# Optimization experiments

Measured on AMD Instinct MI355X. Metric: run time of the kernel, lower is better.

Reference implementation:

```python
import jax, jax.numpy as jnp
import numpy as np

NUM_BINS = 256
BN_EPS = 1e-5


def setup_inputs() -> dict:
    key = jax.random.key(0)
    ks = jax.random.split(key, 16)
    B, C, H, W = 16, 64, 256, 256
    x = jax.random.uniform(ks[0], (B, C, H, W), dtype=jnp.float32) * 255.0
    return {
        "x": x,
        "conv1_w": jax.random.normal(ks[1], (C, C), dtype=jnp.float32) * 0.05,
        "conv1_b": jax.random.normal(ks[2], (C,), dtype=jnp.float32) * 0.05,
        "bn1_gamma": jax.random.uniform(ks[3], (C,), dtype=jnp.float32) + 0.5,
        "bn1_beta": jax.random.normal(ks[4], (C,), dtype=jnp.float32) * 0.05,
        "bn1_mean": jax.random.normal(ks[5], (C,), dtype=jnp.float32) * 0.05,
        "bn1_var": jax.random.uniform(ks[6], (C,), dtype=jnp.float32) + 0.5,
        "conv2_w": jax.random.normal(ks[7], (1, C), dtype=jnp.float32) * 0.05,
        "conv2_b": jax.random.normal(ks[8], (1,), dtype=jnp.float32) * 0.05,
        "bn2_gamma": jax.random.uniform(ks[9], (1,), dtype=jnp.float32) + 0.5,
        "bn2_beta": jax.random.normal(ks[10], (1,), dtype=jnp.float32) * 0.05,
        "bn2_mean": jax.random.normal(ks[11], (1,), dtype=jnp.float32) * 0.05,
        "bn2_var": jax.random.uniform(ks[12], (1,), dtype=jnp.float32) + 0.5,
    }


def _histc_argmax(x):
    # Replicates torch.histc(v, bins=NUM_BINS, min=0, max=255) per (b, c)
    # followed by argmax over bins. Out-of-range values are ignored by histc.
    B, C, H, W = x.shape
    flat = x.reshape(B * C, H * W)
    in_range = (flat >= 0.0) & (flat <= 255.0)
    # histc bin index: floor((v - min) * bins / (max - min)); v == max -> last bin
    idx = jnp.clip((flat * (NUM_BINS / 255.0)).astype(jnp.int32), 0, NUM_BINS - 1)
    rows = jnp.arange(B * C)[:, None]
    hist = jnp.zeros((B * C, NUM_BINS), dtype=jnp.float32).at[rows, idx].add(
        in_range.astype(jnp.float32)
    )
    return hist.argmax(axis=-1).reshape(B, C)  # [B, C] dominant bin indices


def _bn(a, gamma, beta, mean, var):
    inv = gamma * jax.lax.rsqrt(var + BN_EPS)
    return a * inv[None, :, None, None] + (beta - mean * inv)[None, :, None, None]


def reference(x, conv1_w, conv1_b, bn1_gamma, bn1_beta, bn1_mean, bn1_var,
              conv2_w, conv2_b, bn2_gamma, bn2_beta, bn2_mean, bn2_var):
    bin_size = 256 // NUM_BINS  # == 1 for default num_bins
    dominant = _histc_argmax(x)  # [B, C]
    # per-pixel bin index: torch's x.float() // bin_size then .long()
    pixel_bins = jnp.floor(x / bin_size).astype(jnp.int32)  # [B, C, H, W]
    att = (pixel_bins != dominant[:, :, None, None]).astype(x.dtype)
    # conv1 (1x1) -> bn1 -> relu
    a = jnp.einsum('bchw,oc->bohw', att, conv1_w) + conv1_b[None, :, None, None]
    a = jax.nn.relu(_bn(a, bn1_gamma, bn1_beta, bn1_mean, bn1_var))
    # conv2 (1x1, C->1) -> bn2 -> sigmoid
    a = jnp.einsum('bchw,oc->bohw', a, conv2_w) + conv2_b[None, :, None, None]
    a = jax.nn.sigmoid(_bn(a, bn2_gamma, bn2_beta, bn2_mean, bn2_var))
    return x * a
```

## Files before the change

kernel.cpp:

```cpp
#include <hip/hip_runtime.h>
#include <stdint.h>

#define CCH 64
#define HWPIX 65536
#define NBINS 256

typedef float f4 __attribute__((ext_vector_type(4)));


__global__ __launch_bounds__(64) void precomp_kernel(
    const float* __restrict__ w1, const float* __restrict__ b1,
    const float* __restrict__ g1, const float* __restrict__ be1,
    const float* __restrict__ m1, const float* __restrict__ v1,
    const float* __restrict__ w2, const float* __restrict__ b2,
    const float* __restrict__ g2, const float* __restrict__ be2,
    const float* __restrict__ m2, const float* __restrict__ v2,
    float* __restrict__ ws)
{
    int o = threadIdx.x;
    float inv1 = g1[o] * rsqrtf(v1[o] + 1e-5f);
    float S = 0.f;
    for (int c = 0; c < CCH; ++c) S += w1[o * CCH + c];
    float beta1p = be1[o] - m1[o] * inv1;
    float base_pre = (S + b1[o]) * inv1 + beta1p;
    for (int c = 0; c < CCH; ++c) ws[1024 + o * CCH + c] = w1[o * CCH + c] * inv1;
    ws[5120 + o] = base_pre;
    float w2o = w2[o];
    ws[5184 + o] = w2o;
    float t = fmaxf(base_pre, 0.f) * w2o;
    #pragma unroll
    for (int off = 32; off > 0; off >>= 1) t += __shfl_down(t, off, 64);
    if (o == 0) {
        float inv2 = g2[0] * rsqrtf(v2[0] + 1e-5f);
        float beta2p = be2[0] - m2[0] * inv2;
        float z = (t + b2[0]) * inv2 + beta2p;
        ws[5248] = inv2;
        ws[5249] = beta2p;
        ws[5250] = b2[0];
        ws[5251] = 1.f / (1.f + expf(-z));
    }
    __syncthreads();
    {
        int c = o;
        float t1 = 0.f;
        for (int oo = 0; oo < CCH; ++oo) {
            float acc = ws[5120 + oo] - ws[1024 + oo * CCH + c];
            t1 += fmaxf(acc, 0.f) * ws[5184 + oo];
        }
        float z = (t1 + ws[5250]) * ws[5248] + ws[5249];
        ws[5312 + c] = 1.f / (1.f + expf(-z));
    }
}

__global__ __launch_bounds__(64) void precomp2_kernel(float* __restrict__ ws)
{
    int c1 = blockIdx.x, c2 = threadIdx.x;
    float t = 0.f;
    for (int o = 0; o < CCH; ++o) {
        float acc = ws[5120 + o] - ws[1024 + o * CCH + c1] - ws[1024 + o * CCH + c2];
        t += fmaxf(acc, 0.f) * ws[5184 + o];
    }
    float z = (t + ws[5250]) * ws[5248] + ws[5249];
    ws[8192 + c1 * CCH + c2] = 1.f / (1.f + expf(-z));
}

__global__ __launch_bounds__(256) void hist_kernel(
    const float* __restrict__ x, int* __restrict__ dom)
{
    __shared__ unsigned h[16][NBINS + 1];
    __shared__ unsigned long long red[NBINS];
    int tid = threadIdx.x;
    const float4* xp = (const float4*)(x + (size_t)blockIdx.x * HWPIX);

    for (int i = tid; i < 16 * (NBINS + 1); i += 256) ((unsigned*)h)[i] = 0;
    __syncthreads();

    unsigned* hmine = h[tid >> 4];
    const float scale = 256.0f / 255.0f;
    #pragma unroll 4
    for (int t = 0; t < HWPIX / 4 / 256; ++t) {
        float4 v = xp[t * 256 + tid];
        float vv[4] = {v.x, v.y, v.z, v.w};
        #pragma unroll
        for (int j = 0; j < 4; ++j) {
            float f = vv[j];
            if (f >= 0.f && f <= 255.f) {
                int bi = (int)(f * scale);
                bi = bi > NBINS - 1 ? NBINS - 1 : bi;
                atomicAdd(&hmine[bi], 1u);
            }
        }
    }
    __syncthreads();

    unsigned cnt = 0;
    #pragma unroll
    for (int k = 0; k < 16; ++k) cnt += h[k][tid];
    red[tid] = ((unsigned long long)cnt << 32) | (unsigned)(NBINS - 1 - tid);
    __syncthreads();
    #pragma unroll
    for (int s = 128; s > 0; s >>= 1) {
        if (tid < s) {
            unsigned long long a = red[tid], b = red[tid + s];
            red[tid] = a > b ? a : b;
        }
        __syncthreads();
    }
    if (tid == 0) dom[blockIdx.x] = (NBINS - 1) - (int)(red[0] & 0xffffffffu);
}

__global__ __launch_bounds__(256, 8) void main_kernel(
    const float* __restrict__ x, const float* __restrict__ ws,
    const int* __restrict__ dom, float* __restrict__ out)
{
    __shared__ __align__(16) float tile[CCH][68];
    __shared__ unsigned pm[4][CCH];
    __shared__ float ss[CCH];
    __shared__ float df[CCH];

    int tid = threadIdx.x;
    int b = blockIdx.x >> 10;
    int p04 = (blockIdx.x & 1023) << 4;

    if (tid < CCH) df[tid] = (float)dom[b * CCH + tid];

    const f4* xb4 = (const f4*)(x + ((size_t)b << 22));
    #pragma unroll
    for (int k = 0; k < 4; ++k) {
        int id = (k << 8) + tid;
        int c = id >> 4, col = id & 15;
        f4 v = xb4[((size_t)c << 14) + p04 + col];
        *(f4*)&tile[c][col << 2] = v;
    }
    __syncthreads();

    {
        int part = tid >> 6, px = tid & 63;
        unsigned mloc = 0;
        #pragma unroll
        for (int cc = 0; cc < 16; ++cc) {
            int c = (part << 4) | cc;
            float v = tile[c][px];
            float d = df[c];
            mloc |= (unsigned)(v >= d && v < d + 1.0f) << cc;
        }
        pm[part][px] = mloc;
    }
    __syncthreads();

    if (tid < CCH) {
        int px = tid;
        unsigned long long m = (unsigned long long)pm[0][px]
            | ((unsigned long long)pm[1][px] << 16)
            | ((unsigned long long)pm[2][px] << 32)
            | ((unsigned long long)pm[3][px] << 48);
        float s;
        if (m == 0ull) {
            s = ws[5251];
        } else {
            int c1 = __builtin_ctzll(m);
            unsigned long long r1 = m & (m - 1);
            if (r1 == 0ull) {
                s = ws[5312 + c1];
            } else {
                int c2 = __builtin_ctzll(r1);
                unsigned long long r2 = r1 & (r1 - 1);
                if (r2 == 0ull) {
                    s = ws[8192 + (c1 << 6) + c2];
                } else {
                    float t = 0.f;
                    for (int o = 0; o < CCH; ++o) {
                        float acc = ws[5120 + o];
                        unsigned long long mm = m;
                        const float* row = ws + 1024 + (o << 6);
                        while (mm) {
                            int c = __builtin_ctzll(mm);
                            mm &= mm - 1;
                            acc -= row[c];
                        }
                        t += fmaxf(acc, 0.f) * ws[5184 + o];
                    }
                    float z = (t + ws[5250]) * ws[5248] + ws[5249];
                    s = 1.f / (1.f + expf(-z));
                }
            }
        }
        ss[px] = s;
    }
    __syncthreads();

    f4* ob4 = (f4*)(out + ((size_t)b << 22));
    #pragma unroll
    for (int k = 0; k < 4; ++k) {
        int id = (k << 8) + tid;
        int c = id >> 4, col = id & 15;
        f4 v = *(const f4*)&tile[c][col << 2];
        f4 sv = *(const f4*)&ss[col << 2];
        v *= sv;
        __builtin_nontemporal_store(v, &ob4[((size_t)c << 14) + p04 + col]);
    }
}

extern "C" void kernel_launch(void* const* d_in, const int* in_sizes, int n_in,
                              void* d_out, int out_size, void* d_ws, size_t ws_size,
                              hipStream_t stream) {
    const float* x   = (const float*)d_in[0];
    const float* w1  = (const float*)d_in[1];
    const float* b1  = (const float*)d_in[2];
    const float* g1  = (const float*)d_in[3];
    const float* be1 = (const float*)d_in[4];
    const float* m1  = (const float*)d_in[5];
    const float* v1  = (const float*)d_in[6];
    const float* w2  = (const float*)d_in[7];
    const float* b2  = (const float*)d_in[8];
    const float* g2  = (const float*)d_in[9];
    const float* be2 = (const float*)d_in[10];
    const float* m2  = (const float*)d_in[11];
    const float* v2  = (const float*)d_in[12];

    float* ws  = (float*)d_ws;
    int*   dom = (int*)d_ws;
    float* outp = (float*)d_out;

    int B = in_sizes[0] / (CCH * HWPIX);

    precomp_kernel<<<1, 64, 0, stream>>>(w1, b1, g1, be1, m1, v1,
                                         w2, b2, g2, be2, m2, v2, ws);
    precomp2_kernel<<<CCH, 64, 0, stream>>>(ws);
    hist_kernel<<<B * CCH, 256, 0, stream>>>(x, dom);
    main_kernel<<<B * (HWPIX / 64), 256, 0, stream>>>(x, ws, dom, outp);
}
```

Baseline: 167.9 us.

## Make main kernel persistent over 8 chunks with double-buffered async LDS loads

Each block of the main kernel now handles 8 consecutive 64-pixel chunks instead of one, loading the next chunk straight into LDS with global_load_lds while the current chunk is processed. The channel-mask computation is also reworked so 64 threads each scan all 64 channels in one pass, replacing the two-stage partial-mask reduction. The intent is to hide global load latency and spread per-block setup cost over more work. The cost is 8x fewer blocks (2048), which may reduce occupancy and latency hiding across the GPU, and most lanes sit idle during the mask phase.

```diff
diff --git a/kernel.cpp b/kernel.cpp
--- a/kernel.cpp
+++ b/kernel.cpp
@@ -6,6 +6,11 @@
 #define NBINS 256
 
 typedef float f4 __attribute__((ext_vector_type(4)));
+
+#define GLDS16(gp, lp)                                                        \
+    __builtin_amdgcn_global_load_lds(                                         \
+        (const __attribute__((address_space(1))) uint32_t*)(gp),              \
+        (__attribute__((address_space(3))) uint32_t*)(lp), 16, 0, 0)
 
 
 __global__ __launch_bounds__(64) void precomp_kernel(
@@ -109,95 +114,105 @@
     if (tid == 0) dom[blockIdx.x] = (NBINS - 1) - (int)(red[0] & 0xffffffffu);
 }
 
-__global__ __launch_bounds__(256, 8) void main_kernel(
+__global__ __launch_bounds__(256) void main_kernel(
     const float* __restrict__ x, const float* __restrict__ ws,
     const int* __restrict__ dom, float* __restrict__ out)
 {
-    __shared__ __align__(16) float tile[CCH][68];
-    __shared__ unsigned pm[4][CCH];
-    __shared__ float ss[CCH];
+    __shared__ __align__(16) float tile[2][CCH * 64];
+    __shared__ float ss[64];
     __shared__ float df[CCH];
 
     int tid = threadIdx.x;
-    int b = blockIdx.x >> 10;
-    int p04 = (blockIdx.x & 1023) << 4;
-
-    if (tid < CCH) df[tid] = (float)dom[b * CCH + tid];
-
-    const f4* xb4 = (const f4*)(x + ((size_t)b << 22));
+    int img = blockIdx.x >> 7;
+    int c0  = (blockIdx.x & 127) << 3;
+
+    const f4* xb4 = (const f4*)(x + ((size_t)img << 22));
+    f4*       ob4 = (f4*)(out + ((size_t)img << 22));
+
     #pragma unroll
     for (int k = 0; k < 4; ++k) {
         int id = (k << 8) + tid;
         int c = id >> 4, col = id & 15;
-        f4 v = xb4[((size_t)c << 14) + p04 + col];
-        *(f4*)&tile[c][col << 2] = v;
-    }
-    __syncthreads();
-
-    {
-        int part = tid >> 6, px = tid & 63;
-        unsigned mloc = 0;
+        GLDS16(xb4 + ((size_t)c << 14) + (c0 << 4) + col, &tile[0][id << 2]);
+    }
+    if (tid < CCH) df[tid] = (float)dom[img * CCH + tid];
+    __syncthreads();
+
+    for (int i = 0; i < 8; ++i) {
+        int cur = i & 1;
+        int j = c0 + i;
+        if (i < 7) {
+            int jn = j + 1;
+            #pragma unroll
+            for (int k = 0; k < 4; ++k) {
+                int id = (k << 8) + tid;
+                int c = id >> 4, col = id & 15;
+                GLDS16(xb4 + ((size_t)c << 14) + (jn << 4) + col,
+                       &tile[cur ^ 1][id << 2]);
+            }
+            asm volatile("s_waitcnt vmcnt(4)" ::: "memory");
+        } else {
+            asm volatile("s_waitcnt vmcnt(0)" ::: "memory");
+        }
+        __builtin_amdgcn_s_barrier();
+
+        if ((tid & 63) < 16) {
+            int px = ((tid >> 6) << 4) | (tid & 15);
+            const float* tc = &tile[cur][0];
+            unsigned long long m = 0ull;
+            #pragma unroll
+            for (int c = 0; c < CCH; ++c) {
+                float v = tc[(c << 6) | px];
+                float d = df[c];
+                m |= (unsigned long long)(v >= d && v < d + 1.0f) << c;
+            }
+            float s;
+            if (m == 0ull) {
+                s = ws[5251];
+            } else {
+                int c1 = __builtin_ctzll(m);
+                unsigned long long r1 = m & (m - 1);
+                if (r1 == 0ull) {
+                    s = ws[5312 + c1];
+                } else {
+                    int c2 = __builtin_ctzll(r1);
+                    unsigned long long r2 = r1 & (r1 - 1);
+                    if (r2 == 0ull) {
+                        s = ws[8192 + (c1 << 6) + c2];
+                    } else {
+                        float t = 0.f;
+                        for (int o = 0; o < CCH; ++o) {
+                            float acc = ws[5120 + o];
+                            unsigned long long mm = m;
+                            const float* row = ws + 1024 + (o << 6);
+                            while (mm) {
+                                int c = __builtin_ctzll(mm);
+                                mm &= mm - 1;
+                                acc -= row[c];
+                            }
+                            t += fmaxf(acc, 0.f) * ws[5184 + o];
+                        }
+                        float z = (t + ws[5250]) * ws[5248] + ws[5249];
+                        s = 1.f / (1.f + expf(-z));
+                    }
+                }
+            }
+            ss[px] = s;
+        }
+        asm volatile("s_waitcnt lgkmcnt(0)" ::: "memory");
+        __builtin_amdgcn_s_barrier();
+
         #pragma unroll
-        for (int cc = 0; cc < 16; ++cc) {
-            int c = (part << 4) | cc;
-            float v = tile[c][px];
-            float d = df[c];
-            mloc |= (unsigned)(v >= d && v < d + 1.0f) << cc;
-        }
-        pm[part][px] = mloc;
-    }
-    __syncthreads();
-
-    if (tid < CCH) {
-        int px = tid;
-        unsigned long long m = (unsigned long long)pm[0][px]
-            | ((unsigned long long)pm[1][px] << 16)
-            | ((unsigned long long)pm[2][px] << 32)
-            | ((unsigned long long)pm[3][px] << 48);
-        float s;
-        if (m == 0ull) {
-            s = ws[5251];
-        } else {
-            int c1 = __builtin_ctzll(m);
-            unsigned long long r1 = m & (m - 1);
-            if (r1 == 0ull) {
-                s = ws[5312 + c1];
-            } else {
-                int c2 = __builtin_ctzll(r1);
-                unsigned long long r2 = r1 & (r1 - 1);
-                if (r2 == 0ull) {
-                    s = ws[8192 + (c1 << 6) + c2];
-                } else {
-                    float t = 0.f;
-                    for (int o = 0; o < CCH; ++o) {
-                        float acc = ws[5120 + o];
-                        unsigned long long mm = m;
-                        const float* row = ws + 1024 + (o << 6);
-                        while (mm) {
-                            int c = __builtin_ctzll(mm);
-                            mm &= mm - 1;
-                            acc -= row[c];
-                        }
-                        t += fmaxf(acc, 0.f) * ws[5184 + o];
-                    }
-                    float z = (t + ws[5250]) * ws[5248] + ws[5249];
-                    s = 1.f / (1.f + expf(-z));
-                }
-            }
-        }
-        ss[px] = s;
-    }
-    __syncthreads();
-
-    f4* ob4 = (f4*)(out + ((size_t)b << 22));
-    #pragma unroll
-    for (int k = 0; k < 4; ++k) {
-        int id = (k << 8) + tid;
-        int c = id >> 4, col = id & 15;
-        f4 v = *(const f4*)&tile[c][col << 2];
-        f4 sv = *(const f4*)&ss[col << 2];
-        v *= sv;
-        __builtin_nontemporal_store(v, &ob4[((size_t)c << 14) + p04 + col]);
+        for (int k = 0; k < 4; ++k) {
+            int id = (k << 8) + tid;
+            int c = id >> 4, col = id & 15;
+            f4 v = *(const f4*)&tile[cur][id << 2];
+            f4 sv = *(const f4*)&ss[col << 2];
+            v *= sv;
+            __builtin_nontemporal_store(v, &ob4[((size_t)c << 14) + (j << 4) + col]);
+        }
+        asm volatile("s_waitcnt lgkmcnt(0)" ::: "memory");
+        __builtin_amdgcn_s_barrier();
     }
 }
 
@@ -228,5 +243,5 @@
                                          w2, b2, g2, be2, m2, v2, ws);
     precomp2_kernel<<<CCH, 64, 0, stream>>>(ws);
     hist_kernel<<<B * CCH, 256, 0, stream>>>(x, dom);
-    main_kernel<<<B * (HWPIX / 64), 256, 0, stream>>>(x, ws, dom, outp);
-}
+    main_kernel<<<B * 128, 256, 0, stream>>>(x, ws, dom, outp);
+}
```

Result: slower. 266.6 us (+58.7%).

## Keep pixel data in registers and reverse block order in main kernel

Applied to the files above, without the earlier changes.

The main kernel no longer stages the 64x64 input tile in shared memory. Each thread now holds four float4 values in registers, builds per-channel match bitmasks, and ORs them through small shared arrays before scaling and storing directly from registers. Blocks are also processed in reverse order, so the last images read by the histogram kernel are likely still in cache (L2/MALL). This cuts shared-memory traffic and LDS footprint, and may improve cache reuse of x, in exchange for more registers per thread.

```diff
diff --git a/kernel.cpp b/kernel.cpp
--- a/kernel.cpp
+++ b/kernel.cpp
@@ -6,6 +6,7 @@
 #define NBINS 256
 
 typedef float f4 __attribute__((ext_vector_type(4)));
+typedef unsigned u32x4 __attribute__((ext_vector_type(4)));
 
 
 __global__ __launch_bounds__(64) void precomp_kernel(
@@ -113,47 +114,56 @@
     const float* __restrict__ x, const float* __restrict__ ws,
     const int* __restrict__ dom, float* __restrict__ out)
 {
-    __shared__ __align__(16) float tile[CCH][68];
-    __shared__ unsigned pm[4][CCH];
-    __shared__ float ss[CCH];
-    __shared__ float df[CCH];
+    __shared__ unsigned pmlo[16][64];
+    __shared__ unsigned pmhi[16][64];
+    __shared__ float ss[64];
 
     int tid = threadIdx.x;
-    int b = blockIdx.x >> 10;
-    int p04 = (blockIdx.x & 1023) << 4;
-
-    if (tid < CCH) df[tid] = (float)dom[b * CCH + tid];
-
-    const f4* xb4 = (const f4*)(x + ((size_t)b << 22));
-    #pragma unroll
-    for (int k = 0; k < 4; ++k) {
-        int id = (k << 8) + tid;
-        int c = id >> 4, col = id & 15;
-        f4 v = xb4[((size_t)c << 14) + p04 + col];
-        *(f4*)&tile[c][col << 2] = v;
-    }
-    __syncthreads();
-
-    {
-        int part = tid >> 6, px = tid & 63;
-        unsigned mloc = 0;
+    int rc = (gridDim.x - 1) - blockIdx.x;
+    int img = rc >> 10;
+    int jc  = rc & 1023;
+    int g   = tid >> 4;
+    int col = tid & 15;
+    int px0 = col << 2;
+
+    const f4* xb4 = (const f4*)(x + ((size_t)img << 22));
+    f4*       ob4 = (f4*)(out + ((size_t)img << 22));
+    size_t base = ((size_t)jc << 4) + col;
+
+    f4 v0 = xb4[((size_t)(g     ) << 14) + base];
+    f4 v1 = xb4[((size_t)(g + 16) << 14) + base];
+    f4 v2 = xb4[((size_t)(g + 32) << 14) + base];
+    f4 v3 = xb4[((size_t)(g + 48) << 14) + base];
+
+    const int* domi = dom + img * CCH;
+    float d0 = (float)domi[g];
+    float d1 = (float)domi[g + 16];
+    float d2 = (float)domi[g + 32];
+    float d3 = (float)domi[g + 48];
+
+    unsigned lo[4], hi[4];
+    #pragma unroll
+    for (int j = 0; j < 4; ++j) {
+        unsigned l = 0, h = 0;
+        l |= (unsigned)(v0[j] >= d0 && v0[j] < d0 + 1.0f) << g;
+        l |= (unsigned)(v1[j] >= d1 && v1[j] < d1 + 1.0f) << (g + 16);
+        h |= (unsigned)(v2[j] >= d2 && v2[j] < d2 + 1.0f) << g;
+        h |= (unsigned)(v3[j] >= d3 && v3[j] < d3 + 1.0f) << (g + 16);
+        lo[j] = l; hi[j] = h;
+    }
+    *(u32x4*)&pmlo[g][px0] = *(u32x4*)lo;
+    *(u32x4*)&pmhi[g][px0] = *(u32x4*)hi;
+    __syncthreads();
+
+    if (tid < 64) {
+        int px = tid;
+        unsigned mlo = 0, mhi = 0;
         #pragma unroll
-        for (int cc = 0; cc < 16; ++cc) {
-            int c = (part << 4) | cc;
-            float v = tile[c][px];
-            float d = df[c];
-            mloc |= (unsigned)(v >= d && v < d + 1.0f) << cc;
-        }
-        pm[part][px] = mloc;
-    }
-    __syncthreads();
-
-    if (tid < CCH) {
-        int px = tid;
-        unsigned long long m = (unsigned long long)pm[0][px]
-            | ((unsigned long long)pm[1][px] << 16)
-            | ((unsigned long long)pm[2][px] << 32)
-            | ((unsigned long long)pm[3][px] << 48);
+        for (int gg = 0; gg < 16; ++gg) {
+            mlo |= pmlo[gg][px];
+            mhi |= pmhi[gg][px];
+        }
+        unsigned long long m = ((unsigned long long)mhi << 32) | mlo;
         float s;
         if (m == 0ull) {
             s = ws[5251];
@@ -189,16 +199,12 @@
     }
     __syncthreads();
 
-    f4* ob4 = (f4*)(out + ((size_t)b << 22));
-    #pragma unroll
-    for (int k = 0; k < 4; ++k) {
-        int id = (k << 8) + tid;
-        int c = id >> 4, col = id & 15;
-        f4 v = *(const f4*)&tile[c][col << 2];
-        f4 sv = *(const f4*)&ss[col << 2];
-        v *= sv;
-        __builtin_nontemporal_store(v, &ob4[((size_t)c << 14) + p04 + col]);
-    }
+    f4 sv = *(const f4*)&ss[px0];
+    v0 *= sv; v1 *= sv; v2 *= sv; v3 *= sv;
+    __builtin_nontemporal_store(v0, &ob4[((size_t)(g     ) << 14) + base]);
+    __builtin_nontemporal_store(v1, &ob4[((size_t)(g + 16) << 14) + base]);
+    __builtin_nontemporal_store(v2, &ob4[((size_t)(g + 32) << 14) + base]);
+    __builtin_nontemporal_store(v3, &ob4[((size_t)(g + 48) << 14) + base]);
 }
 
 extern "C" void kernel_launch(void* const* d_in, const int* in_sizes, int n_in,
@@ -228,5 +234,5 @@
                                          w2, b2, g2, be2, m2, v2, ws);
     precomp2_kernel<<<CCH, 64, 0, stream>>>(ws);
     hist_kernel<<<B * CCH, 256, 0, stream>>>(x, dom);
-    main_kernel<<<B * (HWPIX / 64), 256, 0, stream>>>(x, ws, dom, outp);
-}
+    main_kernel<<<B * 1024, 256, 0, stream>>>(x, ws, dom, outp);
+}
```

New measurement: 170.7 us. Within noise of the previous version (+1.7%).
